# Kernel tuning notes

Measured on AMD Instinct MI355X. Metric: run time of the kernel, lower is better.

The kernel has to match this reference:

```python
import jax, jax.numpy as jnp
import numpy as np

N = 8388608
WEIGHT = 0.1
TARGET_ITERS = 30.0
MAX_ITERS = 100


def setup_inputs() -> dict:
    key = jax.random.key(0)
    k1, k2 = jax.random.split(key)
    c_real = jax.random.normal(k1, (N,), dtype=jnp.float32)
    c_imag = jax.random.normal(k2, (N,), dtype=jnp.float32)
    return {"c_real": c_real, "c_imag": c_imag}


def _escape_time(c_real, c_imag):
    zeros = jnp.zeros_like(c_real)
    active0 = jnp.ones(c_real.shape, dtype=bool)
    max_f = jnp.float32(MAX_ITERS)

    def body(i, st):
        zr, zi, zr_prev, zi_prev, iters, active = st
        zr_new = zr * zr - zi * zi + c_real
        zi_new = 2.0 * zr * zi + c_imag
        mag_sq = zr_new * zr_new + zi_new * zi_new
        escaped = mag_sq > 4.0
        # cycle detection (skipped on first iteration, matching `if i > 0`)
        dr = jnp.abs(zr_new - zr_prev)
        di = jnp.abs(zi_new - zi_prev)
        in_cycle = (dr < 1e-6) & (di < 1e-6) & active & (i > 0)
        iters = jnp.where(in_cycle, max_f, iters)
        active = active & ~in_cycle
        just_escaped = escaped & active
        iters = jnp.where(just_escaped, (i + 1).astype(jnp.float32), iters)
        active = active & ~escaped
        return (zr_new, zi_new, zr_new, zi_new, iters, active)

    st = (zeros, zeros, zeros, zeros, zeros, active0)
    _, _, _, _, iters, _ = jax.lax.fori_loop(0, MAX_ITERS, body, st)
    iters = jnp.where(iters == 0.0, max_f, iters)
    return iters


def reference(c_real, c_imag):
    escape_iters = _escape_time(c_real, c_imag)
    normalized_distance = jnp.abs(escape_iters - TARGET_ITERS) / TARGET_ITERS
    return WEIGHT * jnp.mean(normalized_distance)
```

## Files before the change

kernel.cpp:

```cpp
#include <hip/hip_runtime.h>

#define MAXIT  100
#define TARGET 30.0f
#define WEIGHT 0.1f
#define EPB    1024
#define TPB    256
#define R0     4
#define RSTEP  16
#define ND_INSET ((100.0f - TARGET) * (1.0f / TARGET))
#define INV_T  (1.0f / TARGET)

__device__ __forceinline__ void body4(float& zr, float& zi, float cr, float ci,
                                      float fb, float& nd, bool& alive) {
  float t0  = __builtin_fmaf(-zi, zi, cr);
  float zr1 = __builtin_fmaf(zr, zr, t0);
  float zi1 = __builtin_fmaf(zr + zr, zi, ci);

  float t1  = __builtin_fmaf(-zi1, zi1, cr);
  float zr2 = __builtin_fmaf(zr1, zr1, t1);
  float zi2 = __builtin_fmaf(zr1 + zr1, zi1, ci);

  float t2  = __builtin_fmaf(-zi2, zi2, cr);
  float zr3 = __builtin_fmaf(zr2, zr2, t2);
  float zi3 = __builtin_fmaf(zr2 + zr2, zi2, ci);

  float t3  = __builtin_fmaf(-zi3, zi3, cr);
  float zr4 = __builtin_fmaf(zr3, zr3, t3);
  float zi4 = __builtin_fmaf(zr3 + zr3, zi3, ci);

  float m4  = __builtin_fmaf(zr4, zr4, zi4 * zi4);
  zr = zr4; zi = zi4;

  if ((m4 > 4.0f) & alive) {
    bool e1 = __builtin_fmaf(zr1, zr1, zi1 * zi1) > 4.0f;
    bool e2 = __builtin_fmaf(zr2, zr2, zi2 * zi2) > 4.0f;
    bool e3 = __builtin_fmaf(zr3, zr3, zi3 * zi3) > 4.0f;
    float f = fb + 4.0f;
    if (e3) f = fb + 3.0f;
    if (e2) f = fb + 2.0f;
    if (e1) f = fb + 1.0f;
    f = fminf(f, 100.0f);
    nd += fabsf(f - TARGET) * INV_T;
    alive = false;
  }
}

__device__ __forceinline__ bool inside_main_regions(float cr, float ci) {
  float ci2 = ci * ci;
  float xq  = cr - 0.25f;
  float q   = __builtin_fmaf(xq, xq, ci2);
  bool card = q * (q + xq) < 0.25f * ci2;
  float xb  = cr + 1.0f;
  bool bulb = __builtin_fmaf(xb, xb, ci2) < 0.0625f;
  return card | bulb;
}

__global__ __launch_bounds__(TPB) void escape_partial(
    const float* __restrict__ crg, const float* __restrict__ cig,
    float* __restrict__ partial, int n) {
  __shared__ float4 q[EPB];
  __shared__ int scount;
  __shared__ float sm[4];

  const int tid  = threadIdx.x;
  const int lane = tid & 63;
  const int wid  = tid >> 6;
  const int blockBase = blockIdx.x * EPB;

  float nd = 0.0f;
  float eZr[4], eZi[4], eCr[4], eCi[4];
  bool  eAl[4];

  const bool fullBlock = (blockBase + EPB) <= n;
  float4 vcr, vci;
  if (fullBlock) {
    vcr = reinterpret_cast<const float4*>(crg + blockBase)[tid];
    vci = reinterpret_cast<const float4*>(cig + blockBase)[tid];
  } else {
    int b = blockBase + 4 * tid;
    vcr.x = (b + 0 < n) ? crg[b + 0] : 9.0f;  vci.x = (b + 0 < n) ? cig[b + 0] : 9.0f;
    vcr.y = (b + 1 < n) ? crg[b + 1] : 9.0f;  vci.y = (b + 1 < n) ? cig[b + 1] : 9.0f;
    vcr.z = (b + 2 < n) ? crg[b + 2] : 9.0f;  vci.z = (b + 2 < n) ? cig[b + 2] : 9.0f;
    vcr.w = (b + 3 < n) ? crg[b + 3] : 9.0f;  vci.w = (b + 3 < n) ? cig[b + 3] : 9.0f;
  }
  const float crs[4] = {vcr.x, vcr.y, vcr.z, vcr.w};
  const float cis[4] = {vci.x, vci.y, vci.z, vci.w};
  const bool  vld[4] = {
    fullBlock || (blockBase + 4 * tid + 0 < n),
    fullBlock || (blockBase + 4 * tid + 1 < n),
    fullBlock || (blockBase + 4 * tid + 2 < n),
    fullBlock || (blockBase + 4 * tid + 3 < n)};

  #pragma unroll
  for (int k = 0; k < 4; ++k) {
    float c_r = crs[k], c_i = cis[k];
    bool inside = inside_main_regions(c_r, c_i) & vld[k];
    if (inside) nd += ND_INSET;
    float zr = 0.0f, zi = 0.0f;
    bool alive = vld[k] & (!inside);
    body4(zr, zi, c_r, c_i, 0.0f, nd, alive);
    eAl[k] = alive; eZr[k] = zr; eZi[k] = zi; eCr[k] = c_r; eCi[k] = c_i;
  }

  if (tid == 0) scount = 0;
  __syncthreads();
  #pragma unroll
  for (int k = 0; k < 4; ++k) {
    unsigned long long bal = __ballot(eAl[k]);
    int cnt = __popcll(bal);
    if (cnt) {
      int wbase = 0;
      if (lane == 0) wbase = atomicAdd(&scount, cnt);
      wbase = __shfl(wbase, 0, 64);
      if (eAl[k]) {
        int pos = wbase + __popcll(bal & ((1ull << lane) - 1ull));
        q[pos] = make_float4(eZr[k], eZi[k], eCr[k], eCi[k]);
      }
    }
  }
  __syncthreads();
  int S = scount;
  int rot = 0;

  for (int base = R0; base < MAXIT && S > 0; base += RSTEP) {
    rot = (rot + 64) & (TPB - 1);
    const int effTid = (tid + rot) & (TPB - 1);
    const float fb = (float)base;
    #pragma unroll
    for (int k = 0; k < 4; ++k) {
      eAl[k] = false;
      int j = k * TPB + effTid;
      if (j < S) {
        float4 e = q[j];
        float zr = e.x, zi = e.y, c_r = e.z, c_i = e.w;
        bool alive = true;
        body4(zr, zi, c_r, c_i, fb,         nd, alive);
        body4(zr, zi, c_r, c_i, fb +  4.0f, nd, alive);
        body4(zr, zi, c_r, c_i, fb +  8.0f, nd, alive);
        body4(zr, zi, c_r, c_i, fb + 12.0f, nd, alive);
        eAl[k] = alive; eZr[k] = zr; eZi[k] = zi; eCr[k] = c_r; eCi[k] = c_i;
      }
    }
    __syncthreads();
    if (tid == 0) scount = 0;
    __syncthreads();
    #pragma unroll
    for (int k = 0; k < 4; ++k) {
      unsigned long long bal = __ballot(eAl[k]);
      int cnt = __popcll(bal);
      if (cnt) {
        int wbase = 0;
        if (lane == 0) wbase = atomicAdd(&scount, cnt);
        wbase = __shfl(wbase, 0, 64);
        if (eAl[k]) {
          int pos = wbase + __popcll(bal & ((1ull << lane) - 1ull));
          q[pos] = make_float4(eZr[k], eZi[k], eCr[k], eCi[k]);
        }
      }
    }
    __syncthreads();
    S = scount;
  }

  {
    int mine = 0;
    #pragma unroll
    for (int k = 0; k < 4; ++k) if (k * TPB + tid < S) ++mine;
    nd += (float)mine * ND_INSET;
  }

  for (int off = 32; off > 0; off >>= 1) nd += __shfl_down(nd, off, 64);
  if (lane == 0) sm[wid] = nd;
  __syncthreads();
  if (tid == 0) partial[blockIdx.x] = sm[0] + sm[1] + sm[2] + sm[3];
}

__global__ __launch_bounds__(256) void reduce_final(
    const float* __restrict__ partial, int nparts,
    float* __restrict__ out, float scale) {
  float s = 0.0f;
  int n4 = nparts >> 2;
  const float4* p4 = reinterpret_cast<const float4*>(partial);
  for (int i = threadIdx.x; i < n4; i += 256) {
    float4 v = p4[i];
    s += (v.x + v.y) + (v.z + v.w);
  }
  for (int i = (n4 << 2) + threadIdx.x; i < nparts; i += 256) s += partial[i];
  for (int off = 32; off > 0; off >>= 1) s += __shfl_down(s, off, 64);
  __shared__ float sm[4];
  int lane = threadIdx.x & 63, wid = threadIdx.x >> 6;
  if (lane == 0) sm[wid] = s;
  __syncthreads();
  if (threadIdx.x == 0)
    out[0] = (sm[0] + sm[1] + sm[2] + sm[3]) * scale;
}

extern "C" void kernel_launch(void* const* d_in, const int* in_sizes, int n_in,
                              void* d_out, int out_size, void* d_ws, size_t ws_size,
                              hipStream_t stream) {
  const float* cr = (const float*)d_in[0];
  const float* ci = (const float*)d_in[1];
  int n = in_sizes[0];
  int blocks = (n + EPB - 1) / EPB;
  float* partial = (float*)d_ws;

  escape_partial<<<blocks, TPB, 0, stream>>>(cr, ci, partial, n);
  reduce_final<<<1, 256, 0, stream>>>(partial, blocks, (float*)d_out,
                                      WEIGHT / (float)n);
}
```

Measured before the change: 122.1 us.

## Fuse final reduction via last-block atomics and double iteration chunk per compaction

Drops the separate reduce kernel. Each block atomically adds its partial sum into one of 64 slots, and the last block to finish, detected through an atomic counter, sums the slots and writes the output. A memset of the workspace is added to clear the counter. The compaction step also doubles from 16 to 32 iterations, which halves the number of queue compactions and barriers but wastes more work on lanes that escape early within a chunk.

```diff
diff --git a/kernel.cpp b/kernel.cpp
--- a/kernel.cpp
+++ b/kernel.cpp
@@ -6,7 +6,8 @@
 #define EPB    1024
 #define TPB    256
 #define R0     4
-#define RSTEP  16
+#define RSTEP  32
+#define NSLOTS 64
 #define ND_INSET ((100.0f - TARGET) * (1.0f / TARGET))
 #define INV_T  (1.0f / TARGET)
 
@@ -57,7 +58,8 @@
 
 __global__ __launch_bounds__(TPB) void escape_partial(
     const float* __restrict__ crg, const float* __restrict__ cig,
-    float* __restrict__ partial, int n) {
+    unsigned int* __restrict__ counter, float* __restrict__ slots,
+    float* __restrict__ out, int n, int nblocks, float scale) {
   __shared__ float4 q[EPB];
   __shared__ int scount;
   __shared__ float sm[4];
@@ -134,10 +136,9 @@
         float4 e = q[j];
         float zr = e.x, zi = e.y, c_r = e.z, c_i = e.w;
         bool alive = true;
-        body4(zr, zi, c_r, c_i, fb,         nd, alive);
-        body4(zr, zi, c_r, c_i, fb +  4.0f, nd, alive);
-        body4(zr, zi, c_r, c_i, fb +  8.0f, nd, alive);
-        body4(zr, zi, c_r, c_i, fb + 12.0f, nd, alive);
+        #pragma unroll
+        for (int b = 0; b < 8; ++b)
+          body4(zr, zi, c_r, c_i, fb + 4.0f * (float)b, nd, alive);
         eAl[k] = alive; eZr[k] = zr; eZi[k] = zi; eCr[k] = c_r; eCi[k] = c_i;
       }
     }
@@ -172,27 +173,23 @@
   for (int off = 32; off > 0; off >>= 1) nd += __shfl_down(nd, off, 64);
   if (lane == 0) sm[wid] = nd;
   __syncthreads();
-  if (tid == 0) partial[blockIdx.x] = sm[0] + sm[1] + sm[2] + sm[3];
-}
-
-__global__ __launch_bounds__(256) void reduce_final(
-    const float* __restrict__ partial, int nparts,
-    float* __restrict__ out, float scale) {
-  float s = 0.0f;
-  int n4 = nparts >> 2;
-  const float4* p4 = reinterpret_cast<const float4*>(partial);
-  for (int i = threadIdx.x; i < n4; i += 256) {
-    float4 v = p4[i];
-    s += (v.x + v.y) + (v.z + v.w);
-  }
-  for (int i = (n4 << 2) + threadIdx.x; i < nparts; i += 256) s += partial[i];
-  for (int off = 32; off > 0; off >>= 1) s += __shfl_down(s, off, 64);
-  __shared__ float sm[4];
-  int lane = threadIdx.x & 63, wid = threadIdx.x >> 6;
-  if (lane == 0) sm[wid] = s;
-  __syncthreads();
-  if (threadIdx.x == 0)
-    out[0] = (sm[0] + sm[1] + sm[2] + sm[3]) * scale;
+
+  if (tid == 0) {
+    float bs = sm[0] + sm[1] + sm[2] + sm[3];
+    atomicAdd(&slots[blockIdx.x & (NSLOTS - 1)], bs);
+    __threadfence();
+    unsigned int old = atomicAdd(counter, 1u);
+    sm[0] = (old == (unsigned int)(nblocks - 1)) ? 1.0f : 0.0f;
+  }
+  __syncthreads();
+  if (sm[0] != 0.0f) {
+    __threadfence();
+    if (tid < NSLOTS) {
+      float v = atomicAdd(&slots[tid], 0.0f);
+      for (int off = 32; off > 0; off >>= 1) v += __shfl_down(v, off, 64);
+      if (tid == 0) out[0] = v * scale;
+    }
+  }
 }
 
 extern "C" void kernel_launch(void* const* d_in, const int* in_sizes, int n_in,
@@ -202,9 +199,11 @@
   const float* ci = (const float*)d_in[1];
   int n = in_sizes[0];
   int blocks = (n + EPB - 1) / EPB;
-  float* partial = (float*)d_ws;
-
-  escape_partial<<<blocks, TPB, 0, stream>>>(cr, ci, partial, n);
-  reduce_final<<<1, 256, 0, stream>>>(partial, blocks, (float*)d_out,
-                                      WEIGHT / (float)n);
-}
+  unsigned int* counter = (unsigned int*)d_ws;
+  float* slots = (float*)((char*)d_ws + 256);
+
+  hipMemsetAsync(d_ws, 0, 1024, stream);
+  escape_partial<<<blocks, TPB, 0, stream>>>(cr, ci, counter, slots,
+                                             (float*)d_out, n, blocks,
+                                             WEIGHT / (float)n);
+}
```

Result: slower. 276.0 us (+126.1%).
